# Kernel tuning notes

Measured on AMD Instinct MI355X. Metric: run time of the kernel, lower is better.

## Reference

```python
import jax, jax.numpy as jnp
import numpy as np

N, E, D, K = 32768, 16384, 4, 8          # nodes, hyperedges, edges/node, nodes/edge
IN_DIM, OUT_DIM, EDGE_DIM, NUM_HEADS = 128, 128, 64, 8


def setup_inputs() -> dict:
    key = jax.random.key(0)
    ks = jax.random.split(key, 16)
    s_in = 1.0 / np.sqrt(IN_DIM)
    s_out = 1.0 / np.sqrt(OUT_DIM)
    s_edge = 1.0 / np.sqrt(EDGE_DIM)
    return {
        "x": jax.random.normal(ks[0], (N, IN_DIM), jnp.float32),
        "edge_attr": jax.random.normal(ks[1], (E, EDGE_DIM), jnp.float32),
        "node_edges": jax.random.randint(ks[2], (N, D), 0, E),   # hyperedges containing each node
        "edge_nodes": jax.random.randint(ks[3], (E, K), 0, N),   # nodes inside each hyperedge
        "W_lin": jax.random.normal(ks[4], (OUT_DIM, IN_DIM), jnp.float32) * s_in,
        "W_edge": jax.random.normal(ks[5], (OUT_DIM, EDGE_DIM), jnp.float32) * s_edge,
        "Wq": jax.random.normal(ks[6], (OUT_DIM, OUT_DIM), jnp.float32) * s_out,
        "Wk": jax.random.normal(ks[7], (OUT_DIM, OUT_DIM), jnp.float32) * s_out,
        "Wv": jax.random.normal(ks[8], (OUT_DIM, OUT_DIM), jnp.float32) * s_out,
        "bq": jnp.zeros((OUT_DIM,), jnp.float32),
        "bk": jnp.zeros((OUT_DIM,), jnp.float32),
        "bv": jnp.zeros((OUT_DIM,), jnp.float32),
        "Wo": jax.random.normal(ks[9], (OUT_DIM, OUT_DIM), jnp.float32) * s_out,
        "bo": jnp.zeros((OUT_DIM,), jnp.float32),
    }


def reference(x, edge_attr, node_edges, edge_nodes,
              W_lin, W_edge, Wq, Wk, Wv, bq, bk, bv, Wo, bo):
    n, out_dim = x.shape[0], W_lin.shape[0]
    hd = out_dim // NUM_HEADS
    L = node_edges.shape[1] * edge_nodes.shape[1]  # D*K keys per node

    Wh = x @ W_lin.T                               # [N, out]
    We = edge_attr @ W_edge.T                      # [E, out]

    u_idx = edge_nodes[node_edges]                 # [N, D, K] neighbor node ids
    vals = Wh[u_idx]                               # [N, D, K, out]
    keys = vals + We[node_edges][:, :, None, :]    # key = Wh[u] + We[e]
    keys = keys.reshape(n, L, out_dim)
    vals = vals.reshape(n, L, out_dim)

    # torch nn.MultiheadAttention: single query per node (query = Wh[v])
    q = (Wh @ Wq.T + bq).reshape(n, NUM_HEADS, hd)
    k = (keys @ Wk.T + bk).reshape(n, L, NUM_HEADS, hd)
    v = (vals @ Wv.T + bv).reshape(n, L, NUM_HEADS, hd)

    scores = jnp.einsum('nhd,nlhd->nhl', q, k) / jnp.sqrt(jnp.asarray(hd, q.dtype))
    attn = jax.nn.softmax(scores, axis=-1)         # [N, H, L]
    ctx = jnp.einsum('nhl,nlhd->nhd', attn, v).reshape(n, out_dim)
    out = ctx @ Wo.T + bo
    return jax.nn.relu(out)
```

## Files before the change

kernel.cpp:

```cpp
#include <hip/hip_runtime.h>

#define N_NODES 32768
#define N_EDGES 16384
#define DEG 4
#define KPE 8
#define DIM 128
#define EDIM 64

typedef float f32x4 __attribute__((ext_vector_type(4)));
typedef __bf16 bf16x8 __attribute__((ext_vector_type(8)));
typedef __bf16 bf16x2 __attribute__((ext_vector_type(2)));
typedef unsigned short u16x8 __attribute__((ext_vector_type(8)));
typedef unsigned int u32;
typedef unsigned int u32x4 __attribute__((ext_vector_type(4)));

static __device__ __forceinline__ unsigned short f2bf(float f) {
  union { float f; unsigned int u; } v; v.f = f;
  unsigned int r = (v.u + 0x7FFFu + ((v.u >> 16) & 1u)) >> 16;
  return (unsigned short)r;
}
static __device__ __forceinline__ float bflo(unsigned int v) {
  union { unsigned int u; float f; } x; x.u = v << 16; return x.f;
}
static __device__ __forceinline__ float bfhi(unsigned int v) {
  union { unsigned int u; float f; } x; x.u = v & 0xffff0000u; return x.f;
}

#if __has_builtin(__builtin_amdgcn_fdot2_f32_bf16)
static __device__ __forceinline__ float dot2bf(unsigned int a, unsigned int b, float c) {
  return __builtin_amdgcn_fdot2_f32_bf16(
      __builtin_bit_cast(bf16x2, a), __builtin_bit_cast(bf16x2, b), c, false);
}
#else
static __device__ __forceinline__ float dot2bf(unsigned int a, unsigned int b, float c) {
  c = fmaf(bflo(a), bflo(b), c);
  return fmaf(bfhi(a), bfhi(b), c);
}
#endif

__global__ __launch_bounds__(256) void wprep_kernel(
    const float* __restrict__ Wq, const float* __restrict__ Wk,
    const float* __restrict__ Wv, const float* __restrict__ Wlin,
    const float* __restrict__ Wedge, const float* __restrict__ Wo,
    unsigned short* __restrict__ CW, unsigned short* __restrict__ CWE,
    unsigned short* __restrict__ Wob)
{
  int id = blockIdx.x * 256 + threadIdx.x;
  if (id < 384 * 128) {
    int j = id >> 7, i = id & 127;
    const float* wrow; float scale = 1.0f;
    if (j < 128)      { wrow = Wq + j * 128; scale = 0.25f; }
    else if (j < 256) { wrow = Wk + (j - 128) * 128; }
    else              { wrow = Wv + (j - 256) * 128; }
    float s = 0.f;
    #pragma unroll 8
    for (int m = 0; m < 128; ++m) s += wrow[m] * Wlin[m * 128 + i];
    CW[id] = f2bf(s * scale);
  } else if (id < 384 * 128 + 128 * 64) {
    int id2 = id - 384 * 128; int j = id2 >> 6, t = id2 & 63;
    float s = 0.f;
    #pragma unroll 8
    for (int m = 0; m < 128; ++m) s += Wk[j * 128 + m] * Wedge[m * 64 + t];
    CWE[id2] = f2bf(s);
  } else if (id < 384 * 128 + 128 * 64 + 128 * 128) {
    int id3 = id - (384 * 128 + 128 * 64);
    Wob[id3] = f2bf(Wo[id3]);
  }
}

__global__ __launch_bounds__(256) void g12_kernel(
    const float* __restrict__ x, const unsigned short* __restrict__ CW,
    const float* __restrict__ bq, const float* __restrict__ bv,
    unsigned short* __restrict__ qb, unsigned short* __restrict__ Kb,
    unsigned short* __restrict__ Vb,
    const float* __restrict__ ea, const unsigned short* __restrict__ CWE,
    const float* __restrict__ bk, unsigned short* __restrict__ WeKb)
{
  const int wave = threadIdx.x >> 6, lane = threadIdx.x & 63;
  const int r16 = lane & 15, quad = lane >> 4;

  if (blockIdx.x < 512) {
    const int m0 = blockIdx.x * 64 + wave * 16;
    u16x8 av[4];
    const float* arow = x + (size_t)(m0 + r16) * DIM + quad * 8;
    #pragma unroll
    for (int kk = 0; kk < 4; ++kk) {
      float4 a0 = *(const float4*)(arow + kk * 32);
      float4 a1 = *(const float4*)(arow + kk * 32 + 4);
      u16x8 au;
      au[0] = f2bf(a0.x); au[1] = f2bf(a0.y); au[2] = f2bf(a0.z); au[3] = f2bf(a0.w);
      au[4] = f2bf(a1.x); au[5] = f2bf(a1.y); au[6] = f2bf(a1.z); au[7] = f2bf(a1.w);
      av[kk] = au;
    }
    #pragma unroll
    for (int g = 0; g < 6; ++g) {
      f32x4 acc[4];
      const f32x4 z = {0.f, 0.f, 0.f, 0.f};
      acc[0] = z; acc[1] = z; acc[2] = z; acc[3] = z;
      #pragma unroll
      for (int kk = 0; kk < 4; ++kk) {
        #pragma unroll
        for (int s = 0; s < 4; ++s) {
          u16x8 bu = *(const u16x8*)(CW + (size_t)(g * 64 + s * 16 + r16) * DIM + kk * 32 + quad * 8);
          acc[s] = __builtin_amdgcn_mfma_f32_16x16x32_bf16(
              __builtin_bit_cast(bf16x8, av[kk]), __builtin_bit_cast(bf16x8, bu), acc[s], 0, 0, 0);
        }
      }
      const int arr = g >> 1;
      const int colbase = (g & 1) * 64;
      unsigned short* dst = arr == 0 ? qb : (arr == 1 ? Kb : Vb);
      #pragma unroll
      for (int s = 0; s < 4; ++s) {
        int j = colbase + s * 16 + r16;
        float bias = arr == 0 ? 0.25f * bq[j] : (arr == 2 ? bv[j] : 0.f);
        #pragma unroll
        for (int r = 0; r < 4; ++r) {
          int m = m0 + quad * 4 + r;
          dst[(size_t)m * DIM + j] = f2bf(acc[s][r] + bias);
        }
      }
    }
  } else {
    const int idx = blockIdx.x - 512;
    const int m0 = (idx >> 1) * 64 + wave * 16;
    const int n0 = (idx & 1) * 64;
    f32x4 acc[4];
    const f32x4 z = {0.f, 0.f, 0.f, 0.f};
    acc[0] = z; acc[1] = z; acc[2] = z; acc[3] = z;
    const float* arow = ea + (size_t)(m0 + r16) * EDIM + quad * 8;
    #pragma unroll
    for (int kk = 0; kk < 2; ++kk) {
      float4 a0 = *(const float4*)(arow + kk * 32);
      float4 a1 = *(const float4*)(arow + kk * 32 + 4);
      u16x8 au;
      au[0] = f2bf(a0.x); au[1] = f2bf(a0.y); au[2] = f2bf(a0.z); au[3] = f2bf(a0.w);
      au[4] = f2bf(a1.x); au[5] = f2bf(a1.y); au[6] = f2bf(a1.z); au[7] = f2bf(a1.w);
      bf16x8 av = __builtin_bit_cast(bf16x8, au);
      #pragma unroll
      for (int s = 0; s < 4; ++s) {
        u16x8 bu = *(const u16x8*)(CWE + (size_t)(n0 + s * 16 + r16) * EDIM + kk * 32 + quad * 8);
        acc[s] = __builtin_amdgcn_mfma_f32_16x16x32_bf16(
            av, __builtin_bit_cast(bf16x8, bu), acc[s], 0, 0, 0);
      }
    }
    #pragma unroll
    for (int s = 0; s < 4; ++s) {
      int j = n0 + s * 16 + r16;
      float bias = bk[j];
      #pragma unroll
      for (int r = 0; r < 4; ++r) {
        int m = m0 + quad * 4 + r;
        WeKb[(size_t)m * DIM + j] = f2bf(acc[s][r] + bias);
      }
    }
  }
}

__global__ __launch_bounds__(64, 4) void attn_kernel(
    const unsigned short* __restrict__ qb, const unsigned short* __restrict__ Kb,
    const unsigned short* __restrict__ Vb, const unsigned short* __restrict__ WeKb,
    const int* __restrict__ nedges, const int* __restrict__ enodes,
    unsigned short* __restrict__ ctxb)
{
  __shared__ __align__(16) unsigned char ldsK[32 * 272];
  __shared__ __align__(16) unsigned char ldsE[4 * 272];
  __shared__ __align__(16) float ldsP[8][36];
  const int lane = threadIdx.x;
  const int n = blockIdx.x;
  const int l = lane & 31, half = lane >> 5;
  const int h = lane >> 3;
  const int c0 = lane * 2;

  int4 e4 = *(const int4*)(nedges + (size_t)n * DEG);
  int4 m0 = *(const int4*)(enodes + (size_t)e4.x * KPE);
  int4 m1 = *(const int4*)(enodes + (size_t)e4.x * KPE + 4);
  int4 m2 = *(const int4*)(enodes + (size_t)e4.y * KPE);
  int4 m3 = *(const int4*)(enodes + (size_t)e4.y * KPE + 4);
  int4 m4 = *(const int4*)(enodes + (size_t)e4.z * KPE);
  int4 m5 = *(const int4*)(enodes + (size_t)e4.z * KPE + 4);
  int4 m6 = *(const int4*)(enodes + (size_t)e4.w * KPE);
  int4 m7 = *(const int4*)(enodes + (size_t)e4.w * KPE + 4);

#define STAGE(ldsdst, table, row) do {                                          \
    const u32* gp_ = (const u32*)((table) + (size_t)(row) * DIM) + lane;        \
    __builtin_amdgcn_global_load_lds(                                           \
        (const __attribute__((address_space(1))) u32*)gp_,                      \
        (__attribute__((address_space(3))) u32*)(ldsdst), 4, 0, 0);             \
  } while (0)
  STAGE(ldsK + 0  * 272, Kb, m0.x); STAGE(ldsK + 1  * 272, Kb, m0.y);
  STAGE(ldsK + 2  * 272, Kb, m0.z); STAGE(ldsK + 3  * 272, Kb, m0.w);
  STAGE(ldsK + 4  * 272, Kb, m1.x); STAGE(ldsK + 5  * 272, Kb, m1.y);
  STAGE(ldsK + 6  * 272, Kb, m1.z); STAGE(ldsK + 7  * 272, Kb, m1.w);
  STAGE(ldsK + 8  * 272, Kb, m2.x); STAGE(ldsK + 9  * 272, Kb, m2.y);
  STAGE(ldsK + 10 * 272, Kb, m2.z); STAGE(ldsK + 11 * 272, Kb, m2.w);
  STAGE(ldsK + 12 * 272, Kb, m3.x); STAGE(ldsK + 13 * 272, Kb, m3.y);
  STAGE(ldsK + 14 * 272, Kb, m3.z); STAGE(ldsK + 15 * 272, Kb, m3.w);
  STAGE(ldsK + 16 * 272, Kb, m4.x); STAGE(ldsK + 17 * 272, Kb, m4.y);
  STAGE(ldsK + 18 * 272, Kb, m4.z); STAGE(ldsK + 19 * 272, Kb, m4.w);
  STAGE(ldsK + 20 * 272, Kb, m5.x); STAGE(ldsK + 21 * 272, Kb, m5.y);
  STAGE(ldsK + 22 * 272, Kb, m5.z); STAGE(ldsK + 23 * 272, Kb, m5.w);
  STAGE(ldsK + 24 * 272, Kb, m6.x); STAGE(ldsK + 25 * 272, Kb, m6.y);
  STAGE(ldsK + 26 * 272, Kb, m6.z); STAGE(ldsK + 27 * 272, Kb, m6.w);
  STAGE(ldsK + 28 * 272, Kb, m7.x); STAGE(ldsK + 29 * 272, Kb, m7.y);
  STAGE(ldsK + 30 * 272, Kb, m7.z); STAGE(ldsK + 31 * 272, Kb, m7.w);
  STAGE(ldsE + 0 * 272, WeKb, e4.x); STAGE(ldsE + 1 * 272, WeKb, e4.y);
  STAGE(ldsE + 2 * 272, WeKb, e4.z); STAGE(ldsE + 3 * 272, WeKb, e4.w);
#undef STAGE

  const u32x4* qp = (const u32x4*)(qb + (size_t)n * DIM + half * 64);
  u32x4 qv[8];
  #pragma unroll
  for (int ch = 0; ch < 8; ++ch) qv[ch] = __builtin_nontemporal_load(qp + ch);

  asm volatile("" ::: "memory");

  u32 vv[32];
#define VLOAD(t, row) vv[t] = *(const u32*)(Vb + (size_t)(row) * DIM + c0)
  VLOAD(0,  m0.x); VLOAD(1,  m0.y); VLOAD(2,  m0.z); VLOAD(3,  m0.w);
  VLOAD(4,  m1.x); VLOAD(5,  m1.y); VLOAD(6,  m1.z); VLOAD(7,  m1.w);
  VLOAD(8,  m2.x); VLOAD(9,  m2.y); VLOAD(10, m2.z); VLOAD(11, m2.w);
  VLOAD(12, m3.x); VLOAD(13, m3.y); VLOAD(14, m3.z); VLOAD(15, m3.w);
  VLOAD(16, m4.x); VLOAD(17, m4.y); VLOAD(18, m4.z); VLOAD(19, m4.w);
  VLOAD(20, m5.x); VLOAD(21, m5.y); VLOAD(22, m5.z); VLOAD(23, m5.w);
  VLOAD(24, m6.x); VLOAD(25, m6.y); VLOAD(26, m6.z); VLOAD(27, m6.w);
  VLOAD(28, m7.x); VLOAD(29, m7.y); VLOAD(30, m7.z); VLOAD(31, m7.w);
#undef VLOAD

  asm volatile("s_waitcnt vmcnt(32)" ::: "memory");

  const unsigned char* krow = ldsK + l * 272 + half * 128;
  const unsigned char* erow = ldsE + (l >> 3) * 272 + half * 128;
  float s[4] = {0.f, 0.f, 0.f, 0.f};
  #pragma unroll
  for (int ch = 0; ch < 8; ++ch) {
    uint4 kc = *(const uint4*)(krow + ch * 16);
    uint4 ec = *(const uint4*)(erow + ch * 16);
    const int hi = ch >> 1;
    float t = s[hi];
    t = dot2bf(qv[ch].x, kc.x, t); t = dot2bf(qv[ch].x, ec.x, t);
    t = dot2bf(qv[ch].y, kc.y, t); t = dot2bf(qv[ch].y, ec.y, t);
    t = dot2bf(qv[ch].z, kc.z, t); t = dot2bf(qv[ch].z, ec.z, t);
    t = dot2bf(qv[ch].w, kc.w, t); t = dot2bf(qv[ch].w, ec.w, t);
    s[hi] = t;
  }

  #pragma unroll
  for (int hi = 0; hi < 4; ++hi) {
    float vmax = s[hi];
    #pragma unroll
    for (int off = 16; off >= 1; off >>= 1)
      vmax = fmaxf(vmax, __shfl_xor(vmax, off, 32));
    float ex = __expf(s[hi] - vmax);
    float sum = ex;
    #pragma unroll
    for (int off = 16; off >= 1; off >>= 1)
      sum += __shfl_xor(sum, off, 32);
    ldsP[half * 4 + hi][l] = ex / sum;
  }

  float a0 = 0.f, a1 = 0.f;
  #pragma unroll
  for (int t = 0; t < 8; ++t) {
    float4 p4 = *(const float4*)&ldsP[h][t * 4];
    a0 = fmaf(p4.x, bflo(vv[t * 4 + 0]), a0); a1 = fmaf(p4.x, bfhi(vv[t * 4 + 0]), a1);
    a0 = fmaf(p4.y, bflo(vv[t * 4 + 1]), a0); a1 = fmaf(p4.y, bfhi(vv[t * 4 + 1]), a1);
    a0 = fmaf(p4.z, bflo(vv[t * 4 + 2]), a0); a1 = fmaf(p4.z, bfhi(vv[t * 4 + 2]), a1);
    a0 = fmaf(p4.w, bflo(vv[t * 4 + 3]), a0); a1 = fmaf(p4.w, bfhi(vv[t * 4 + 3]), a1);
  }
  unsigned int pk = (unsigned int)f2bf(a0) | ((unsigned int)f2bf(a1) << 16);
  __builtin_nontemporal_store(pk, (u32*)(ctxb + (size_t)n * DIM + c0));
}

__global__ __launch_bounds__(256) void g4_kernel(
    const unsigned short* __restrict__ ctxb, const unsigned short* __restrict__ Wob,
    const float* __restrict__ bo, float* __restrict__ out)
{
  const int wave = threadIdx.x >> 6, lane = threadIdx.x & 63;
  const int r16 = lane & 15, quad = lane >> 4;
  const int m0 = blockIdx.x * 64 + wave * 16;
  const int n0 = blockIdx.y * 64;

  f32x4 acc[4];
  const f32x4 z = {0.f, 0.f, 0.f, 0.f};
  acc[0] = z; acc[1] = z; acc[2] = z; acc[3] = z;

  #pragma unroll
  for (int kk = 0; kk < 4; ++kk) {
    u16x8 au = *(const u16x8*)(ctxb + (size_t)(m0 + r16) * DIM + kk * 32 + quad * 8);
    bf16x8 av = __builtin_bit_cast(bf16x8, au);
    #pragma unroll
    for (int s = 0; s < 4; ++s) {
      u16x8 bu = *(const u16x8*)(Wob + (size_t)(n0 + s * 16 + r16) * DIM + kk * 32 + quad * 8);
      acc[s] = __builtin_amdgcn_mfma_f32_16x16x32_bf16(
          av, __builtin_bit_cast(bf16x8, bu), acc[s], 0, 0, 0);
    }
  }

  #pragma unroll
  for (int s = 0; s < 4; ++s) {
    int j = n0 + s * 16 + r16;
    float bias = bo[j];
    #pragma unroll
    for (int r = 0; r < 4; ++r) {
      int m = m0 + quad * 4 + r;
      float v = acc[s][r] + bias;
      out[(size_t)m * DIM + j] = v > 0.f ? v : 0.f;
    }
  }
}

extern "C" void kernel_launch(void* const* d_in, const int* in_sizes, int n_in,
                              void* d_out, int out_size, void* d_ws, size_t ws_size,
                              hipStream_t stream)
{
  const float* x     = (const float*)d_in[0];
  const float* ea    = (const float*)d_in[1];
  const int* nedges  = (const int*)d_in[2];
  const int* enodes  = (const int*)d_in[3];
  const float* Wlin  = (const float*)d_in[4];
  const float* Wedge = (const float*)d_in[5];
  const float* Wq    = (const float*)d_in[6];
  const float* Wk    = (const float*)d_in[7];
  const float* Wv    = (const float*)d_in[8];
  const float* bq    = (const float*)d_in[9];
  const float* bk    = (const float*)d_in[10];
  const float* bv    = (const float*)d_in[11];
  const float* Wo    = (const float*)d_in[12];
  const float* bo    = (const float*)d_in[13];
  float* out = (float*)d_out;

  unsigned short* wsp = (unsigned short*)d_ws;
  unsigned short* CW   = wsp;  wsp += 384 * 128;
  unsigned short* CWE  = wsp;  wsp += 128 * 64;
  unsigned short* Wob  = wsp;  wsp += 128 * 128;
  unsigned short* qb   = wsp;  wsp += (size_t)N_NODES * DIM;
  unsigned short* Kb   = wsp;  wsp += (size_t)N_NODES * DIM;
  unsigned short* Vb   = wsp;  wsp += (size_t)N_NODES * DIM;
  unsigned short* WeKb = wsp;  wsp += (size_t)N_EDGES * DIM;
  unsigned short* ctxb = wsp;  wsp += (size_t)N_NODES * DIM;

  wprep_kernel<<<dim3(288), dim3(256), 0, stream>>>(Wq, Wk, Wv, Wlin, Wedge, Wo, CW, CWE, Wob);
  g12_kernel<<<dim3(1024), dim3(256), 0, stream>>>(x, CW, bq, bv, qb, Kb, Vb, ea, CWE, bk, WeKb);
  attn_kernel<<<dim3(32768), dim3(64), 0, stream>>>(qb, Kb, Vb, WeKb, nedges, enodes, ctxb);
  g4_kernel<<<dim3(512, 2), dim3(256), 0, stream>>>(ctxb, Wob, bo, out);
}
```

Measured before the change: 201.5 us.

## Fuse all four stages into one persistent cooperative kernel with grid syncs

Merges weight prep, the QKV/edge GEMMs, the gather attention and the output GEMM into a single cooperative kernel of 512 blocks. The stages are separated by grid.sync(), and each wave processes attention nodes in a persistent loop. The aim is to remove three kernel launch gaps and let the attention stage run as a persistent schedule. In exchange the grid is capped at 2 blocks per CU, which lowers attention occupancy compared with 4 single-wave blocks, and grid-wide barriers are added. A fallback multi-kernel path is kept, with attention now run as 4-wave blocks.

```diff
diff --git a/kernel.cpp b/kernel.cpp
--- a/kernel.cpp
+++ b/kernel.cpp
@@ -1,4 +1,7 @@
 #include <hip/hip_runtime.h>
+#include <hip/hip_cooperative_groups.h>
+
+namespace cg = cooperative_groups;
 
 #define N_NODES 32768
 #define N_EDGES 16384
@@ -7,6 +10,14 @@
 #define DIM 128
 #define EDIM 64
 
+#define GRID_BLOCKS 512
+#define ATTN_WAVES (GRID_BLOCKS * 4)
+
+#define AOFF_K 0
+#define AOFF_E 8704
+#define AOFF_P 9792
+#define AWAVESZ 10944
+
 typedef float f32x4 __attribute__((ext_vector_type(4)));
 typedef __bf16 bf16x8 __attribute__((ext_vector_type(8)));
 typedef __bf16 bf16x2 __attribute__((ext_vector_type(2)));
@@ -38,14 +49,18 @@
 }
 #endif
 
-__global__ __launch_bounds__(256) void wprep_kernel(
-    const float* __restrict__ Wq, const float* __restrict__ Wk,
+#define GLDS(gp, ldsp, sz) __builtin_amdgcn_global_load_lds(               \
+    (const __attribute__((address_space(1))) u32*)(gp),                    \
+    (__attribute__((address_space(3))) u32*)(ldsp), sz, 0, 0)
+
+
+static __device__ __forceinline__ void wprep_elem(
+    int id, const float* __restrict__ Wq, const float* __restrict__ Wk,
     const float* __restrict__ Wv, const float* __restrict__ Wlin,
     const float* __restrict__ Wedge, const float* __restrict__ Wo,
     unsigned short* __restrict__ CW, unsigned short* __restrict__ CWE,
     unsigned short* __restrict__ Wob)
 {
-  int id = blockIdx.x * 256 + threadIdx.x;
   if (id < 384 * 128) {
     int j = id >> 7, i = id & 127;
     const float* wrow; float scale = 1.0f;
@@ -68,7 +83,8 @@
   }
 }
 
-__global__ __launch_bounds__(256) void g12_kernel(
+static __device__ __forceinline__ void g12_unit(
+    int unit, int wave, int lane,
     const float* __restrict__ x, const unsigned short* __restrict__ CW,
     const float* __restrict__ bq, const float* __restrict__ bv,
     unsigned short* __restrict__ qb, unsigned short* __restrict__ Kb,
@@ -76,11 +92,9 @@
     const float* __restrict__ ea, const unsigned short* __restrict__ CWE,
     const float* __restrict__ bk, unsigned short* __restrict__ WeKb)
 {
-  const int wave = threadIdx.x >> 6, lane = threadIdx.x & 63;
   const int r16 = lane & 15, quad = lane >> 4;
-
-  if (blockIdx.x < 512) {
-    const int m0 = blockIdx.x * 64 + wave * 16;
+  if (unit < 512) {
+    const int m0 = unit * 64 + wave * 16;
     u16x8 av[4];
     const float* arow = x + (size_t)(m0 + r16) * DIM + quad * 8;
     #pragma unroll
@@ -121,7 +135,7 @@
       }
     }
   } else {
-    const int idx = blockIdx.x - 512;
+    const int idx = unit - 512;
     const int m0 = (idx >> 1) * 64 + wave * 16;
     const int n0 = (idx & 1) * 64;
     f32x4 acc[4];
@@ -156,55 +170,47 @@
   }
 }
 
-__global__ __launch_bounds__(64, 4) void attn_kernel(
+static __device__ __forceinline__ void attn_node(
+    int n, unsigned char* __restrict__ abuf, int lane,
     const unsigned short* __restrict__ qb, const unsigned short* __restrict__ Kb,
     const unsigned short* __restrict__ Vb, const unsigned short* __restrict__ WeKb,
     const int* __restrict__ nedges, const int* __restrict__ enodes,
     unsigned short* __restrict__ ctxb)
 {
-  __shared__ __align__(16) unsigned char ldsK[32 * 272];
-  __shared__ __align__(16) unsigned char ldsE[4 * 272];
-  __shared__ __align__(16) float ldsP[8][36];
-  const int lane = threadIdx.x;
-  const int n = blockIdx.x;
+  float* ldsP = (float*)(abuf + AOFF_P);
   const int l = lane & 31, half = lane >> 5;
   const int h = lane >> 3;
   const int c0 = lane * 2;
 
   int4 e4 = *(const int4*)(nedges + (size_t)n * DEG);
-  int4 m0 = *(const int4*)(enodes + (size_t)e4.x * KPE);
-  int4 m1 = *(const int4*)(enodes + (size_t)e4.x * KPE + 4);
-  int4 m2 = *(const int4*)(enodes + (size_t)e4.y * KPE);
-  int4 m3 = *(const int4*)(enodes + (size_t)e4.y * KPE + 4);
-  int4 m4 = *(const int4*)(enodes + (size_t)e4.z * KPE);
-  int4 m5 = *(const int4*)(enodes + (size_t)e4.z * KPE + 4);
-  int4 m6 = *(const int4*)(enodes + (size_t)e4.w * KPE);
-  int4 m7 = *(const int4*)(enodes + (size_t)e4.w * KPE + 4);
-
-#define STAGE(ldsdst, table, row) do {                                          \
-    const u32* gp_ = (const u32*)((table) + (size_t)(row) * DIM) + lane;        \
-    __builtin_amdgcn_global_load_lds(                                           \
-        (const __attribute__((address_space(1))) u32*)gp_,                      \
-        (__attribute__((address_space(3))) u32*)(ldsdst), 4, 0, 0);             \
-  } while (0)
-  STAGE(ldsK + 0  * 272, Kb, m0.x); STAGE(ldsK + 1  * 272, Kb, m0.y);
-  STAGE(ldsK + 2  * 272, Kb, m0.z); STAGE(ldsK + 3  * 272, Kb, m0.w);
-  STAGE(ldsK + 4  * 272, Kb, m1.x); STAGE(ldsK + 5  * 272, Kb, m1.y);
-  STAGE(ldsK + 6  * 272, Kb, m1.z); STAGE(ldsK + 7  * 272, Kb, m1.w);
-  STAGE(ldsK + 8  * 272, Kb, m2.x); STAGE(ldsK + 9  * 272, Kb, m2.y);
-  STAGE(ldsK + 10 * 272, Kb, m2.z); STAGE(ldsK + 11 * 272, Kb, m2.w);
-  STAGE(ldsK + 12 * 272, Kb, m3.x); STAGE(ldsK + 13 * 272, Kb, m3.y);
-  STAGE(ldsK + 14 * 272, Kb, m3.z); STAGE(ldsK + 15 * 272, Kb, m3.w);
-  STAGE(ldsK + 16 * 272, Kb, m4.x); STAGE(ldsK + 17 * 272, Kb, m4.y);
-  STAGE(ldsK + 18 * 272, Kb, m4.z); STAGE(ldsK + 19 * 272, Kb, m4.w);
-  STAGE(ldsK + 20 * 272, Kb, m5.x); STAGE(ldsK + 21 * 272, Kb, m5.y);
-  STAGE(ldsK + 22 * 272, Kb, m5.z); STAGE(ldsK + 23 * 272, Kb, m5.w);
-  STAGE(ldsK + 24 * 272, Kb, m6.x); STAGE(ldsK + 25 * 272, Kb, m6.y);
-  STAGE(ldsK + 26 * 272, Kb, m6.z); STAGE(ldsK + 27 * 272, Kb, m6.w);
-  STAGE(ldsK + 28 * 272, Kb, m7.x); STAGE(ldsK + 29 * 272, Kb, m7.y);
-  STAGE(ldsK + 30 * 272, Kb, m7.z); STAGE(ldsK + 31 * 272, Kb, m7.w);
-  STAGE(ldsE + 0 * 272, WeKb, e4.x); STAGE(ldsE + 1 * 272, WeKb, e4.y);
-  STAGE(ldsE + 2 * 272, WeKb, e4.z); STAGE(ldsE + 3 * 272, WeKb, e4.w);
+  int4 m0i = *(const int4*)(enodes + (size_t)e4.x * KPE);
+  int4 m1i = *(const int4*)(enodes + (size_t)e4.x * KPE + 4);
+  int4 m2i = *(const int4*)(enodes + (size_t)e4.y * KPE);
+  int4 m3i = *(const int4*)(enodes + (size_t)e4.y * KPE + 4);
+  int4 m4i = *(const int4*)(enodes + (size_t)e4.z * KPE);
+  int4 m5i = *(const int4*)(enodes + (size_t)e4.z * KPE + 4);
+  int4 m6i = *(const int4*)(enodes + (size_t)e4.w * KPE);
+  int4 m7i = *(const int4*)(enodes + (size_t)e4.w * KPE + 4);
+
+#define STAGE(off, table, row) GLDS((const u32*)((table) + (size_t)(row) * DIM) + lane, abuf + (off), 4)
+  STAGE(AOFF_K + 0  * 272, Kb, m0i.x); STAGE(AOFF_K + 1  * 272, Kb, m0i.y);
+  STAGE(AOFF_K + 2  * 272, Kb, m0i.z); STAGE(AOFF_K + 3  * 272, Kb, m0i.w);
+  STAGE(AOFF_K + 4  * 272, Kb, m1i.x); STAGE(AOFF_K + 5  * 272, Kb, m1i.y);
+  STAGE(AOFF_K + 6  * 272, Kb, m1i.z); STAGE(AOFF_K + 7  * 272, Kb, m1i.w);
+  STAGE(AOFF_K + 8  * 272, Kb, m2i.x); STAGE(AOFF_K + 9  * 272, Kb, m2i.y);
+  STAGE(AOFF_K + 10 * 272, Kb, m2i.z); STAGE(AOFF_K + 11 * 272, Kb, m2i.w);
+  STAGE(AOFF_K + 12 * 272, Kb, m3i.x); STAGE(AOFF_K + 13 * 272, Kb, m3i.y);
+  STAGE(AOFF_K + 14 * 272, Kb, m3i.z); STAGE(AOFF_K + 15 * 272, Kb, m3i.w);
+  STAGE(AOFF_K + 16 * 272, Kb, m4i.x); STAGE(AOFF_K + 17 * 272, Kb, m4i.y);
+  STAGE(AOFF_K + 18 * 272, Kb, m4i.z); STAGE(AOFF_K + 19 * 272, Kb, m4i.w);
+  STAGE(AOFF_K + 20 * 272, Kb, m5i.x); STAGE(AOFF_K + 21 * 272, Kb, m5i.y);
+  STAGE(AOFF_K + 22 * 272, Kb, m5i.z); STAGE(AOFF_K + 23 * 272, Kb, m5i.w);
+  STAGE(AOFF_K + 24 * 272, Kb, m6i.x); STAGE(AOFF_K + 25 * 272, Kb, m6i.y);
+  STAGE(AOFF_K + 26 * 272, Kb, m6i.z); STAGE(AOFF_K + 27 * 272, Kb, m6i.w);
+  STAGE(AOFF_K + 28 * 272, Kb, m7i.x); STAGE(AOFF_K + 29 * 272, Kb, m7i.y);
+  STAGE(AOFF_K + 30 * 272, Kb, m7i.z); STAGE(AOFF_K + 31 * 272, Kb, m7i.w);
+  STAGE(AOFF_E + 0 * 272, WeKb, e4.x); STAGE(AOFF_E + 1 * 272, WeKb, e4.y);
+  STAGE(AOFF_E + 2 * 272, WeKb, e4.z); STAGE(AOFF_E + 3 * 272, WeKb, e4.w);
 #undef STAGE
 
   const u32x4* qp = (const u32x4*)(qb + (size_t)n * DIM + half * 64);
@@ -216,20 +222,20 @@
 
   u32 vv[32];
 #define VLOAD(t, row) vv[t] = *(const u32*)(Vb + (size_t)(row) * DIM + c0)
-  VLOAD(0,  m0.x); VLOAD(1,  m0.y); VLOAD(2,  m0.z); VLOAD(3,  m0.w);
-  VLOAD(4,  m1.x); VLOAD(5,  m1.y); VLOAD(6,  m1.z); VLOAD(7,  m1.w);
-  VLOAD(8,  m2.x); VLOAD(9,  m2.y); VLOAD(10, m2.z); VLOAD(11, m2.w);
-  VLOAD(12, m3.x); VLOAD(13, m3.y); VLOAD(14, m3.z); VLOAD(15, m3.w);
-  VLOAD(16, m4.x); VLOAD(17, m4.y); VLOAD(18, m4.z); VLOAD(19, m4.w);
-  VLOAD(20, m5.x); VLOAD(21, m5.y); VLOAD(22, m5.z); VLOAD(23, m5.w);
-  VLOAD(24, m6.x); VLOAD(25, m6.y); VLOAD(26, m6.z); VLOAD(27, m6.w);
-  VLOAD(28, m7.x); VLOAD(29, m7.y); VLOAD(30, m7.z); VLOAD(31, m7.w);
+  VLOAD(0,  m0i.x); VLOAD(1,  m0i.y); VLOAD(2,  m0i.z); VLOAD(3,  m0i.w);
+  VLOAD(4,  m1i.x); VLOAD(5,  m1i.y); VLOAD(6,  m1i.z); VLOAD(7,  m1i.w);
+  VLOAD(8,  m2i.x); VLOAD(9,  m2i.y); VLOAD(10, m2i.z); VLOAD(11, m2i.w);
+  VLOAD(12, m3i.x); VLOAD(13, m3i.y); VLOAD(14, m3i.z); VLOAD(15, m3i.w);
+  VLOAD(16, m4i.x); VLOAD(17, m4i.y); VLOAD(18, m4i.z); VLOAD(19, m4i.w);
+  VLOAD(20, m5i.x); VLOAD(21, m5i.y); VLOAD(22, m5i.z); VLOAD(23, m5i.w);
+  VLOAD(24, m6i.x); VLOAD(25, m6i.y); VLOAD(26, m6i.z); VLOAD(27, m6i.w);
+  VLOAD(28, m7i.x); VLOAD(29, m7i.y); VLOAD(30, m7i.z); VLOAD(31, m7i.w);
 #undef VLOAD
 
   asm volatile("s_waitcnt vmcnt(32)" ::: "memory");
 
-  const unsigned char* krow = ldsK + l * 272 + half * 128;
-  const unsigned char* erow = ldsE + (l >> 3) * 272 + half * 128;
+  const unsigned char* krow = abuf + AOFF_K + l * 272 + half * 128;
+  const unsigned char* erow = abuf + AOFF_E + (l >> 3) * 272 + half * 128;
   float s[4] = {0.f, 0.f, 0.f, 0.f};
   #pragma unroll
   for (int ch = 0; ch < 8; ++ch) {
@@ -255,13 +261,13 @@
     #pragma unroll
     for (int off = 16; off >= 1; off >>= 1)
       sum += __shfl_xor(sum, off, 32);
-    ldsP[half * 4 + hi][l] = ex / sum;
+    ldsP[(half * 4 + hi) * 36 + l] = ex / sum;
   }
 
   float a0 = 0.f, a1 = 0.f;
   #pragma unroll
   for (int t = 0; t < 8; ++t) {
-    float4 p4 = *(const float4*)&ldsP[h][t * 4];
+    float4 p4 = *(const float4*)(ldsP + h * 36 + t * 4);
     a0 = fmaf(p4.x, bflo(vv[t * 4 + 0]), a0); a1 = fmaf(p4.x, bfhi(vv[t * 4 + 0]), a1);
     a0 = fmaf(p4.y, bflo(vv[t * 4 + 1]), a0); a1 = fmaf(p4.y, bfhi(vv[t * 4 + 1]), a1);
     a0 = fmaf(p4.z, bflo(vv[t * 4 + 2]), a0); a1 = fmaf(p4.z, bfhi(vv[t * 4 + 2]), a1);
@@ -271,19 +277,18 @@
   __builtin_nontemporal_store(pk, (u32*)(ctxb + (size_t)n * DIM + c0));
 }
 
-__global__ __launch_bounds__(256) void g4_kernel(
+static __device__ __forceinline__ void g4_unit(
+    int unit, int wave, int lane,
     const unsigned short* __restrict__ ctxb, const unsigned short* __restrict__ Wob,
     const float* __restrict__ bo, float* __restrict__ out)
 {
-  const int wave = threadIdx.x >> 6, lane = threadIdx.x & 63;
   const int r16 = lane & 15, quad = lane >> 4;
-  const int m0 = blockIdx.x * 64 + wave * 16;
-  const int n0 = blockIdx.y * 64;
-
+  const int bx = unit & 511, by = unit >> 9;
+  const int m0 = bx * 64 + wave * 16;
+  const int n0 = by * 64;
   f32x4 acc[4];
   const f32x4 z = {0.f, 0.f, 0.f, 0.f};
   acc[0] = z; acc[1] = z; acc[2] = z; acc[3] = z;
-
   #pragma unroll
   for (int kk = 0; kk < 4; ++kk) {
     u16x8 au = *(const u16x8*)(ctxb + (size_t)(m0 + r16) * DIM + kk * 32 + quad * 8);
@@ -295,7 +300,6 @@
           av, __builtin_bit_cast(bf16x8, bu), acc[s], 0, 0, 0);
     }
   }
-
   #pragma unroll
   for (int s = 0; s < 4; ++s) {
     int j = n0 + s * 16 + r16;
@@ -307,6 +311,84 @@
       out[(size_t)m * DIM + j] = v > 0.f ? v : 0.f;
     }
   }
+}
+
+__global__ __launch_bounds__(256, 2) void fused_kernel(
+    const float* __restrict__ x, const float* __restrict__ ea,
+    const int* __restrict__ nedges, const int* __restrict__ enodes,
+    const float* __restrict__ Wlin, const float* __restrict__ Wedge,
+    const float* __restrict__ Wq, const float* __restrict__ Wk,
+    const float* __restrict__ Wv, const float* __restrict__ bq,
+    const float* __restrict__ bk, const float* __restrict__ bv,
+    const float* __restrict__ Wo, const float* __restrict__ bo,
+    unsigned short* __restrict__ CW, unsigned short* __restrict__ CWE,
+    unsigned short* __restrict__ Wob, unsigned short* __restrict__ qb,
+    unsigned short* __restrict__ Kb, unsigned short* __restrict__ Vb,
+    unsigned short* __restrict__ WeKb, unsigned short* __restrict__ ctxb,
+    float* __restrict__ out)
+{
+  __shared__ __align__(16) unsigned char slds[AWAVESZ * 4];
+  cg::grid_group grid = cg::this_grid();
+  const int wave = threadIdx.x >> 6, lane = threadIdx.x & 63;
+
+  wprep_elem(blockIdx.x * 256 + threadIdx.x, Wq, Wk, Wv, Wlin, Wedge, Wo, CW, CWE, Wob);
+  grid.sync();
+
+  for (int unit = blockIdx.x; unit < 1024; unit += GRID_BLOCKS)
+    g12_unit(unit, wave, lane, x, CW, bq, bv, qb, Kb, Vb, ea, CWE, bk, WeKb);
+  grid.sync();
+
+  {
+    unsigned char* abuf = slds + wave * AWAVESZ;
+    const int wv = blockIdx.x * 4 + wave;
+    for (int n = wv; n < N_NODES; n += ATTN_WAVES)
+      attn_node(n, abuf, lane, qb, Kb, Vb, WeKb, nedges, enodes, ctxb);
+  }
+  grid.sync();
+
+  for (int unit = blockIdx.x; unit < 1024; unit += GRID_BLOCKS)
+    g4_unit(unit, wave, lane, ctxb, Wob, bo, out);
+}
+
+__global__ __launch_bounds__(256) void wprep_kernel(
+    const float* __restrict__ Wq, const float* __restrict__ Wk,
+    const float* __restrict__ Wv, const float* __restrict__ Wlin,
+    const float* __restrict__ Wedge, const float* __restrict__ Wo,
+    unsigned short* __restrict__ CW, unsigned short* __restrict__ CWE,
+    unsigned short* __restrict__ Wob)
+{
+  wprep_elem(blockIdx.x * 256 + threadIdx.x, Wq, Wk, Wv, Wlin, Wedge, Wo, CW, CWE, Wob);
+}
+
+__global__ __launch_bounds__(256) void g12_kernel(
+    const float* __restrict__ x, const unsigned short* __restrict__ CW,
+    const float* __restrict__ bq, const float* __restrict__ bv,
+    unsigned short* __restrict__ qb, unsigned short* __restrict__ Kb,
+    unsigned short* __restrict__ Vb,
+    const float* __restrict__ ea, const unsigned short* __restrict__ CWE,
+    const float* __restrict__ bk, unsigned short* __restrict__ WeKb)
+{
+  g12_unit(blockIdx.x, threadIdx.x >> 6, threadIdx.x & 63,
+           x, CW, bq, bv, qb, Kb, Vb, ea, CWE, bk, WeKb);
+}
+
+__global__ __launch_bounds__(256, 2) void attn_kernel(
+    const unsigned short* __restrict__ qb, const unsigned short* __restrict__ Kb,
+    const unsigned short* __restrict__ Vb, const unsigned short* __restrict__ WeKb,
+    const int* __restrict__ nedges, const int* __restrict__ enodes,
+    unsigned short* __restrict__ ctxb)
+{
+  __shared__ __align__(16) unsigned char slds[AWAVESZ * 4];
+  const int wave = threadIdx.x >> 6, lane = threadIdx.x & 63;
+  attn_node(blockIdx.x * 4 + wave, slds + wave * AWAVESZ, lane,
+            qb, Kb, Vb, WeKb, nedges, enodes, ctxb);
+}
+
+__global__ __launch_bounds__(256) void g4_kernel(
+    const unsigned short* __restrict__ ctxb, const unsigned short* __restrict__ Wob,
+    const float* __restrict__ bo, float* __restrict__ out)
+{
+  g4_unit(blockIdx.x, threadIdx.x >> 6, threadIdx.x & 63, ctxb, Wob, bo, out);
 }
 
 extern "C" void kernel_launch(void* const* d_in, const int* in_sizes, int n_in,
@@ -339,8 +421,27 @@
   unsigned short* WeKb = wsp;  wsp += (size_t)N_EDGES * DIM;
   unsigned short* ctxb = wsp;  wsp += (size_t)N_NODES * DIM;
 
+  int maxb = 0;
+  hipError_t qerr = hipOccupancyMaxActiveBlocksPerMultiprocessor(
+      &maxb, (const void*)fused_kernel, 256, 0);
+  bool coop = (qerr == hipSuccess && maxb >= 2);
+
+  if (coop) {
+    void* args[] = {
+      (void*)&x, (void*)&ea, (void*)&nedges, (void*)&enodes,
+      (void*)&Wlin, (void*)&Wedge, (void*)&Wq, (void*)&Wk, (void*)&Wv,
+      (void*)&bq, (void*)&bk, (void*)&bv, (void*)&Wo, (void*)&bo,
+      (void*)&CW, (void*)&CWE, (void*)&Wob, (void*)&qb, (void*)&Kb,
+      (void*)&Vb, (void*)&WeKb, (void*)&ctxb, (void*)&out
+    };
+    hipError_t le = hipLaunchCooperativeKernel((const void*)fused_kernel,
+                                               dim3(GRID_BLOCKS), dim3(256),
+                                               args, 0, stream);
+    if (le == hipSuccess) return;
+  }
+
   wprep_kernel<<<dim3(288), dim3(256), 0, stream>>>(Wq, Wk, Wv, Wlin, Wedge, Wo, CW, CWE, Wob);
   g12_kernel<<<dim3(1024), dim3(256), 0, stream>>>(x, CW, bq, bv, qb, Kb, Vb, ea, CWE, bk, WeKb);
-  attn_kernel<<<dim3(32768), dim3(64), 0, stream>>>(qb, Kb, Vb, WeKb, nedges, enodes, ctxb);
-  g4_kernel<<<dim3(512, 2), dim3(256), 0, stream>>>(ctxb, Wob, bo, out);
-}
+  attn_kernel<<<dim3(8192), dim3(256), 0, stream>>>(qb, Kb, Vb, WeKb, nedges, enodes, ctxb);
+  g4_kernel<<<dim3(1024), dim3(256), 0, stream>>>(ctxb, Wob, bo, out);
+}
```

Result: slower. 207.7 us (+3.1%).
